# Performance work log

Hardware: AMD Instinct MI355X
Metric: run time of the kernel (lower is better)

## Reference

```python
import jax, jax.numpy as jnp
import numpy as np

B, T, D, H = 64, 4096, 256, 341  # hidden = 4*256//3 = 341
TAU, RHO, TV_W = 1.0, 0.3, 0.1
NEG = -1e9
EPS = 1e-6
LN_EPS = 1e-5


def entmax15(x, axis=-1):
    """Exact 1.5-entmax via the sort-based threshold algorithm (Peters et al.)."""
    x = (x - jnp.max(x, axis=axis, keepdims=True)) / 2.0
    xsrt = -jnp.sort(-x, axis=axis)                       # descending
    n = x.shape[axis]
    rho = jnp.arange(1, n + 1, dtype=x.dtype)
    mean = jnp.cumsum(xsrt, axis=axis) / rho
    mean_sq = jnp.cumsum(xsrt * xsrt, axis=axis) / rho
    ss = rho * (mean_sq - mean * mean)
    delta = (1.0 - ss) / rho
    tau = mean - jnp.sqrt(jnp.maximum(delta, 0.0))
    support = jnp.sum((tau <= xsrt).astype(jnp.int32), axis=axis, keepdims=True)
    tau_star = jnp.take_along_axis(tau, support - 1, axis=axis)
    return jnp.square(jnp.maximum(x - tau_star, 0.0))


def setup_inputs() -> dict:
    key = jax.random.key(0)
    k_emb, k_len, k_w1, k_w2 = jax.random.split(key, 4)
    embeddings = jax.random.normal(k_emb, (B, T, D), dtype=jnp.float32)
    # variable-length 0/1 attention mask (lengths in [T//4, T]) -> variable k per row
    lengths = jax.random.randint(k_len, (B,), T // 4, T + 1)
    attn = (jnp.arange(T)[None, :] < lengths[:, None]).astype(jnp.float32)
    ln_gamma = jnp.ones((D,), dtype=jnp.float32)
    ln_beta = jnp.zeros((D,), dtype=jnp.float32)
    W1 = jax.random.normal(k_w1, (D, H), dtype=jnp.float32) / np.sqrt(D)
    b1 = jnp.zeros((H,), dtype=jnp.float32)
    W2 = jax.random.normal(k_w2, (H,), dtype=jnp.float32) / np.sqrt(H)
    b2 = jnp.zeros((), dtype=jnp.float32)
    return {"embeddings": embeddings, "attn": attn, "ln_gamma": ln_gamma,
            "ln_beta": ln_beta, "W1": W1, "b1": b1, "W2": W2, "b2": b2}


def reference(embeddings, attn, ln_gamma, ln_beta, W1, b1, W2, b2):
    # SelectorMLP (dropout off at inference)
    emb = embeddings * attn[..., None]                              # [B,T,D]
    mu = jnp.mean(emb, axis=-1, keepdims=True)
    var = jnp.var(emb, axis=-1, keepdims=True)
    xn = (emb - mu) / jnp.sqrt(var + LN_EPS) * ln_gamma + ln_beta
    hid = jax.nn.gelu(jnp.einsum('btd,dh->bth', xn, W1) + b1, approximate=False)
    scores = jnp.einsum('bth,h->bt', hid, W2) + b2                  # [B,T]
    scores = jnp.where(attn == 0, NEG, scores)

    z = entmax15(scores / TAU, axis=1) * attn                       # soft rationale

    # probabilistic_top_k: gumbel-perturbed variable-k top-k, vectorized
    u = jax.random.uniform(jax.random.key(42), scores.shape, dtype=scores.dtype)
    gumbel = -jnp.log(-jnp.log(u + EPS) + EPS)
    pert = scores * attn + gumbel                                   # [B,T]
    t_eff = jnp.sum(attn, axis=1)                                   # [B]
    k = jnp.clip(jnp.round(RHO * t_eff), 1.0, jnp.maximum(t_eff, 1.0)).astype(jnp.int32)
    srt = -jnp.sort(-pert, axis=1)                                  # descending
    thr = jnp.take_along_axis(srt, (k - 1)[:, None], axis=1)        # k-th largest
    h = (pert >= thr).astype(z.dtype) * attn                        # hard mask

    # straight-through estimator
    g = jax.lax.stop_gradient(h - z) + z

    # total variation regularizer on g within valid region
    dz = jnp.abs(g[:, 1:] - g[:, :-1])
    valid = attn[:, 1:] * attn[:, :-1]
    tv = jnp.mean(jnp.sum(dz * valid, axis=1) / jnp.maximum(jnp.sum(valid, axis=1), 1.0))
    reg = TV_W * tv
    return (z, g, reg)
```

## Files before the change

### kernel.cpp

```cpp
#include <hip/hip_runtime.h>
#include <stdint.h>

#define BB 64
#define TT 4096
#define DD 256
#define HH 341
#define HP 384
#define NEGV (-1e9f)

typedef __attribute__((ext_vector_type(8))) short short8;
typedef __attribute__((ext_vector_type(4))) float f32x4;


__device__ inline float gelu_exact(float x) {
  return 0.5f * x * (1.0f + erff(x * 0.70710678118654752440f));
}

__device__ inline uint32_t rotl32(uint32_t x, int d) { return (x << d) | (x >> (32 - d)); }

__device__ inline uint32_t threefry_bits(uint32_t j) {
  const uint32_t K0 = 0u, K1 = 42u;
  const uint32_t K2 = K0 ^ K1 ^ 0x1BD11BDAu;
  uint32_t x0 = 0u, x1 = j;
  x0 += K0; x1 += K1;
#define TF_RND(r) { x0 += x1; x1 = rotl32(x1, r); x1 ^= x0; }
  TF_RND(13) TF_RND(15) TF_RND(26) TF_RND(6)
  x0 += K1; x1 += K2 + 1u;
  TF_RND(17) TF_RND(29) TF_RND(16) TF_RND(24)
  x0 += K2; x1 += K0 + 2u;
  TF_RND(13) TF_RND(15) TF_RND(26) TF_RND(6)
  x0 += K0; x1 += K1 + 3u;
  TF_RND(17) TF_RND(29) TF_RND(16) TF_RND(24)
  x0 += K1; x1 += K2 + 4u;
  TF_RND(13) TF_RND(15) TF_RND(26) TF_RND(6)
  x0 += K2; x1 += K0 + 5u;
#undef TF_RND
  return x0 ^ x1;
}

__device__ inline void bf16split(float x, short& hi, short& lo) {
  uint32_t u = __float_as_uint(x);
  uint32_t h = (u + 0x7FFFu + ((u >> 16) & 1u)) >> 16;
  float rem = x - __uint_as_float(h << 16);
  uint32_t ur = __float_as_uint(rem);
  uint32_t l = (ur + 0x7FFFu + ((ur >> 16) & 1u)) >> 16;
  hi = (short)h; lo = (short)l;
}

__device__ inline float bred_sum(float v, volatile float* tmp, int tid) {
#pragma unroll
  for (int o = 32; o; o >>= 1) v += __shfl_xor(v, o, 64);
  __syncthreads();
  if ((tid & 63) == 0) tmp[tid >> 6] = v;
  __syncthreads();
  return tmp[0] + tmp[1] + tmp[2] + tmp[3];
}

__device__ inline float bred_max(float v, volatile float* tmp, int tid) {
#pragma unroll
  for (int o = 32; o; o >>= 1) v = fmaxf(v, __shfl_xor(v, o, 64));
  __syncthreads();
  if ((tid & 63) == 0) tmp[tid >> 6] = v;
  __syncthreads();
  return fmaxf(fmaxf(tmp[0], tmp[1]), fmaxf(tmp[2], tmp[3]));
}

__device__ inline int bred_sum_i(int v, volatile int* tmp, int tid) {
#pragma unroll
  for (int o = 32; o; o >>= 1) v += __shfl_xor(v, o, 64);
  __syncthreads();
  if ((tid & 63) == 0) tmp[tid >> 6] = v;
  __syncthreads();
  return tmp[0] + tmp[1] + tmp[2] + tmp[3];
}


__global__ __launch_bounds__(256) void k0_prep(const float* __restrict__ W1,
                                               short* __restrict__ Whi,
                                               short* __restrict__ Wlo) {
  int idx = blockIdx.x * 256 + threadIdx.x;
  int h = idx >> 8, k = idx & 255;
  float v = (h < HH) ? W1[k * HH + h] : 0.0f;
  short hi, lo;
  bf16split(v, hi, lo);
  Whi[idx] = hi;
  Wlo[idx] = lo;
}


__global__ __launch_bounds__(256, 2) void k1_mfma(
    const float* __restrict__ emb, const float* __restrict__ attn,
    const float* __restrict__ gamma, const float* __restrict__ beta,
    const short* __restrict__ Whi, const float* __restrict__ b1,
    const float* __restrict__ W2, const float* __restrict__ b2,
    float* __restrict__ scores) {
  __shared__ short Ahi[16384];
  __shared__ short Alo[16384];

  const int bid = blockIdx.x;
  const int b = bid >> 6;
  const int t0 = (bid & 63) * 64;
  const int tid = threadIdx.x;
  const int w = tid >> 6;
  const int lane = tid & 63;

  if (attn[(size_t)b * TT + t0] == 0.0f) {
    if (tid < 64) scores[(size_t)b * TT + t0 + tid] = NEGV;
    return;
  }

  {
    const int half = lane >> 5;
    const int g = lane & 31;
    const int k0g = g >> 2, qg = g & 3;
    float gg[8], bb[8];
#pragma unroll
    for (int j = 0; j < 8; ++j) { gg[j] = gamma[g * 8 + j]; bb[j] = beta[g * 8 + j]; }

    for (int it = 0; it < 8; ++it) {
      const int il = w * 16 + it * 2 + half;
      const size_t rowoff = (size_t)b * TT + t0 + il;
      const float a = attn[rowoff];
      const float* ep = emb + rowoff * DD + g * 8;
      float x[8];
      {
        float4 xA = *(const float4*)ep;
        float4 xB = *(const float4*)(ep + 4);
        x[0] = xA.x * a; x[1] = xA.y * a; x[2] = xA.z * a; x[3] = xA.w * a;
        x[4] = xB.x * a; x[5] = xB.y * a; x[6] = xB.z * a; x[7] = xB.w * a;
      }
      float s = 0.f, ss = 0.f;
#pragma unroll
      for (int j = 0; j < 8; ++j) { s += x[j]; ss += x[j] * x[j]; }
#pragma unroll
      for (int o = 16; o; o >>= 1) { s += __shfl_xor(s, o, 32); ss += __shfl_xor(ss, o, 32); }
      const float mu = s * (1.0f / DD);
      const float rs = 1.0f / sqrtf(ss * (1.0f / DD) - mu * mu + 1e-5f);

      short8 h8, l8;
#pragma unroll
      for (int j = 0; j < 8; ++j) {
        float y = (x[j] - mu) * rs * gg[j] + bb[j];
        short hi, lo;
        bf16split(y, hi, lo);
        h8[j] = hi; l8[j] = lo;
      }
      const int i15 = it * 2 + half;
      const int slot = w * 512 + k0g * 64 + qg * 16 + (i15 ^ k0g);
      *(short8*)&Ahi[slot * 8] = h8;
      *(short8*)&Alo[slot * 8] = l8;
    }
  }
  __syncthreads();

  const int r = lane & 15, q = lane >> 4;
  f32x4 acc[6][4];
#pragma unroll
  for (int j = 0; j < 6; ++j)
#pragma unroll
    for (int mt = 0; mt < 4; ++mt) acc[j][mt] = (f32x4){0.f, 0.f, 0.f, 0.f};

  int hb[6];
#pragma unroll
  for (int j = 0; j < 6; ++j) hb[j] = ((w * 6 + j) * 16 + r) * 256 + q * 8;

  for (int k0 = 0; k0 < 8; ++k0) {
    short8 ahi[4], alo[4];
#pragma unroll
    for (int mt = 0; mt < 4; ++mt) {
      const int slot = mt * 512 + k0 * 64 + q * 16 + (r ^ k0);
      ahi[mt] = *(const short8*)&Ahi[slot * 8];
      alo[mt] = *(const short8*)&Alo[slot * 8];
    }
#pragma unroll
    for (int j = 0; j < 6; ++j) {
      const short* bp = Whi + hb[j] + k0 * 32;
      short8 bhi = *(const short8*)bp;
      short8 blo = *(const short8*)(bp + HP * DD);
#pragma unroll
      for (int mt = 0; mt < 4; ++mt) {
        acc[j][mt] = __builtin_amdgcn_mfma_f32_16x16x32_bf16(ahi[mt], bhi, acc[j][mt], 0, 0, 0);
        acc[j][mt] = __builtin_amdgcn_mfma_f32_16x16x32_bf16(ahi[mt], blo, acc[j][mt], 0, 0, 0);
        acc[j][mt] = __builtin_amdgcn_mfma_f32_16x16x32_bf16(alo[mt], bhi, acc[j][mt], 0, 0, 0);
      }
    }
  }

  float sacc[4][4];
#pragma unroll
  for (int mt = 0; mt < 4; ++mt)
#pragma unroll
    for (int rr = 0; rr < 4; ++rr) sacc[mt][rr] = 0.f;

#pragma unroll
  for (int j = 0; j < 6; ++j) {
    const int h = (w * 6 + j) * 16 + r;
    const float w2v = (h < HH) ? W2[h] : 0.f;
    const float b1v = (h < HH) ? b1[h] : 0.f;
#pragma unroll
    for (int mt = 0; mt < 4; ++mt)
#pragma unroll
      for (int rr = 0; rr < 4; ++rr) {
        float v = gelu_exact(acc[j][mt][rr] + b1v) * w2v;
        v += __shfl_xor(v, 1, 64);
        v += __shfl_xor(v, 2, 64);
        v += __shfl_xor(v, 4, 64);
        v += __shfl_xor(v, 8, 64);
        sacc[mt][rr] += v;
      }
  }

  __syncthreads();
  float* sred = (float*)Ahi;
  if (r == 0) {
#pragma unroll
    for (int mt = 0; mt < 4; ++mt)
#pragma unroll
      for (int rr = 0; rr < 4; ++rr)
        sred[w * 64 + mt * 16 + q * 4 + rr] = sacc[mt][rr];
  }
  __syncthreads();

  if (tid < 64) {
    float sc = sred[tid] + sred[64 + tid] + sred[128 + tid] + sred[192 + tid] + b2[0];
    float a = attn[(size_t)b * TT + t0 + tid];
    scores[(size_t)b * TT + t0 + tid] = (a != 0.f) ? sc : NEGV;
  }
}


__global__ __launch_bounds__(256) void k2_select(
    const float* __restrict__ attn, float* __restrict__ out, float* __restrict__ row_tv) {
  __shared__ float gs[TT];
  __shared__ float ftmp[4];
  __shared__ int itmp[4];

  const int b = blockIdx.x, tid = threadIdx.x;
  const float* arow = attn + (size_t)b * TT;
  float* zrow = out + (size_t)b * TT;
  float* grow = out + (size_t)BB * TT + (size_t)b * TT;

  float x_loc[16], a_loc[16];
  uint32_t key_loc[16];
  float cnt = 0.0f, mx = -3.4e38f;
#pragma unroll
  for (int i = 0; i < 16; ++i) {
    int t = tid + i * 256;
    float s = grow[t];
    float a = arow[t];
    a_loc[i] = a;
    x_loc[i] = s;
    cnt += a;
    mx = fmaxf(mx, s);
    uint32_t bits = threefry_bits((uint32_t)(b * TT + t));
    float u = __uint_as_float(0x3F800000u | (bits >> 9)) - 1.0f;
    float gum = -logf(1e-6f - logf(u + 1e-6f));
    float pert = (a != 0.0f ? s : 0.0f) + gum;
    uint32_t fb = __float_as_uint(pert);
    uint32_t msk = ((int32_t)fb < 0) ? 0xFFFFFFFFu : 0x80000000u;
    key_loc[i] = fb ^ msk;
  }
  float t_eff = bred_sum(cnt, ftmp, tid);
  mx = bred_max(mx, ftmp, tid);

#pragma unroll
  for (int i = 0; i < 16; ++i) x_loc[i] = (x_loc[i] - mx) * 0.5f;

  float lo = -1.0f, hi = 0.0f;
  for (int it = 0; it < 36; ++it) {
    float mid = 0.5f * (lo + hi);
    float p = 0.0f;
#pragma unroll
    for (int i = 0; i < 16; ++i) {
      float d = x_loc[i] - mid;
      if (d > 0.0f) p = fmaf(d, d, p);
    }
    float f = bred_sum(p, ftmp, tid);
    if (f >= 1.0f) lo = mid; else hi = mid;
  }
  const float tau = 0.5f * (lo + hi);

  float kf = rintf(0.3f * t_eff);
  kf = fminf(fmaxf(kf, 1.0f), fmaxf(t_eff, 1.0f));
  int kk = (int)kf;

  uint32_t prefix = 0u;
  for (int bit = 31; bit >= 0; --bit) {
    uint32_t test = prefix | (1u << bit);
    uint32_t hi_test = test >> bit;
    int c = 0;
#pragma unroll
    for (int i = 0; i < 16; ++i) c += (int)((key_loc[i] >> bit) == hi_test);
    int ct = bred_sum_i(c, itmp, tid);
    if (ct >= kk) prefix = test; else kk -= ct;
  }
  const uint32_t thr = prefix;

#pragma unroll
  for (int i = 0; i < 16; ++i) {
    int t = tid + i * 256;
    float d = x_loc[i] - tau;
    float z = (d > 0.0f) ? d * d : 0.0f;
    z *= a_loc[i];
    float h = (key_loc[i] >= thr) ? a_loc[i] : 0.0f;
    float g = (h - z) + z;
    zrow[t] = z;
    gs[t] = g;
  }
  __syncthreads();

  float tvn = 0.0f, tvd = 0.0f;
#pragma unroll
  for (int i = 0; i < 16; ++i) {
    int t = tid + i * 256;
    grow[t] = gs[t];
    if (t > 0) {
      float valid = arow[t] * arow[t - 1];
      tvn += fabsf(gs[t] - gs[t - 1]) * valid;
      tvd += valid;
    }
  }
  tvn = bred_sum(tvn, ftmp, tid);
  tvd = bred_sum(tvd, ftmp, tid);
  if (tid == 0) row_tv[b] = tvn / fmaxf(tvd, 1.0f);
}


__global__ __launch_bounds__(64) void k3_final(const float* __restrict__ row_tv,
                                               float* __restrict__ out) {
  float v = row_tv[threadIdx.x];
#pragma unroll
  for (int o = 32; o; o >>= 1) v += __shfl_xor(v, o, 64);
  if (threadIdx.x == 0) out[2 * BB * TT] = 0.1f * (v * (1.0f / BB));
}


extern "C" void kernel_launch(void* const* d_in, const int* in_sizes, int n_in,
                              void* d_out, int out_size, void* d_ws, size_t ws_size,
                              hipStream_t stream) {
  const float* emb   = (const float*)d_in[0];
  const float* attn  = (const float*)d_in[1];
  const float* gamma = (const float*)d_in[2];
  const float* beta  = (const float*)d_in[3];
  const float* W1    = (const float*)d_in[4];
  const float* b1    = (const float*)d_in[5];
  const float* W2    = (const float*)d_in[6];
  const float* b2    = (const float*)d_in[7];
  float* out = (float*)d_out;

  float* row_tv = (float*)d_ws;
  short* Whi = (short*)((char*)d_ws + 512);
  short* Wlo = Whi + HP * DD;

  k0_prep<<<dim3(HP * DD / 256), dim3(256), 0, stream>>>(W1, Whi, Wlo);
  k1_mfma<<<dim3(BB * TT / 64), dim3(256), 0, stream>>>(
      emb, attn, gamma, beta, Whi, b1, W2, b2, out + (size_t)BB * TT);
  k2_select<<<dim3(BB), dim3(256), 0, stream>>>(attn, out, row_tv);
  k3_final<<<dim3(1), dim3(64), 0, stream>>>(row_tv, out);
}
```

Measured before the change: 690.2 us.

## Widen MLP kernel to 512 threads, fast GELU, Newton entmax and radix-4 select

The MLP kernel now uses 8 waves per 64-token tile. Each wave owns 3 hidden-column tiles instead of 6, and the cross-lane shuffle reduction runs once per output instead of once per column tile. Exact erff GELU is replaced by an Abramowitz–Stegun polynomial using rcp and fast exp. In the selection kernel, the 36-step bisection for the entmax threshold becomes 18 clamped Newton steps with a fused two-value reduction, and the 32-step bitwise radix select becomes a 16-step radix-4 select with three counts reduced together. These cut ALU work and the number of block barriers, at the cost of small approximation error in GELU and a hard clamp on tau that assumes the threshold stays below -1/64.

```diff
diff --git a/kernel.cpp b/kernel.cpp
--- a/kernel.cpp
+++ b/kernel.cpp
@@ -12,8 +12,18 @@
 typedef __attribute__((ext_vector_type(4))) float f32x4;
 
 
-__device__ inline float gelu_exact(float x) {
-  return 0.5f * x * (1.0f + erff(x * 0.70710678118654752440f));
+__device__ inline float gelu_fast(float x) {
+  const float y = fabsf(x) * 0.70710678118654752440f;
+  const float t = __builtin_amdgcn_rcpf(fmaf(0.3275911f, y, 1.0f));
+  float p = fmaf(1.061405429f, t, -1.453152027f);
+  p = fmaf(p, t, 1.421413741f);
+  p = fmaf(p, t, -0.284496736f);
+  p = fmaf(p, t, 0.254829592f);
+  p *= t;
+  const float e = __expf(-y * y);
+  float er = fmaf(-p, e, 1.0f);
+  er = (x < 0.0f) ? -er : er;
+  return 0.5f * x * (1.0f + er);
 }
 
 __device__ inline uint32_t rotl32(uint32_t x, int d) { return (x << d) | (x >> (32 - d)); }
@@ -65,13 +75,29 @@
   return fmaxf(fmaxf(tmp[0], tmp[1]), fmaxf(tmp[2], tmp[3]));
 }
 
-__device__ inline int bred_sum_i(int v, volatile int* tmp, int tid) {
-#pragma unroll
-  for (int o = 32; o; o >>= 1) v += __shfl_xor(v, o, 64);
-  __syncthreads();
-  if ((tid & 63) == 0) tmp[tid >> 6] = v;
-  __syncthreads();
-  return tmp[0] + tmp[1] + tmp[2] + tmp[3];
+__device__ inline void bred_sum2(float& a, float& b, volatile float* tmp, int tid) {
+#pragma unroll
+  for (int o = 32; o; o >>= 1) { a += __shfl_xor(a, o, 64); b += __shfl_xor(b, o, 64); }
+  __syncthreads();
+  if ((tid & 63) == 0) { int w2 = (tid >> 6) * 2; tmp[w2] = a; tmp[w2 + 1] = b; }
+  __syncthreads();
+  a = tmp[0] + tmp[2] + tmp[4] + tmp[6];
+  b = tmp[1] + tmp[3] + tmp[5] + tmp[7];
+}
+
+__device__ inline void bred3_i(int& a, int& b, int& c, volatile int* tmp, int tid) {
+#pragma unroll
+  for (int o = 32; o; o >>= 1) {
+    a += __shfl_xor(a, o, 64);
+    b += __shfl_xor(b, o, 64);
+    c += __shfl_xor(c, o, 64);
+  }
+  __syncthreads();
+  if ((tid & 63) == 0) { int w3 = (tid >> 6) * 3; tmp[w3] = a; tmp[w3 + 1] = b; tmp[w3 + 2] = c; }
+  __syncthreads();
+  a = tmp[0] + tmp[3] + tmp[6] + tmp[9];
+  b = tmp[1] + tmp[4] + tmp[7] + tmp[10];
+  c = tmp[2] + tmp[5] + tmp[8] + tmp[11];
 }
 
 
@@ -88,7 +114,7 @@
 }
 
 
-__global__ __launch_bounds__(256, 2) void k1_mfma(
+__global__ __launch_bounds__(512, 4) void k1_mfma(
     const float* __restrict__ emb, const float* __restrict__ attn,
     const float* __restrict__ gamma, const float* __restrict__ beta,
     const short* __restrict__ Whi, const float* __restrict__ b1,
@@ -117,8 +143,8 @@
 #pragma unroll
     for (int j = 0; j < 8; ++j) { gg[j] = gamma[g * 8 + j]; bb[j] = beta[g * 8 + j]; }
 
-    for (int it = 0; it < 8; ++it) {
-      const int il = w * 16 + it * 2 + half;
+    for (int it = 0; it < 4; ++it) {
+      const int il = w * 8 + it * 2 + half;
       const size_t rowoff = (size_t)b * TT + t0 + il;
       const float a = attn[rowoff];
       const float* ep = emb + rowoff * DD + g * 8;
@@ -145,8 +171,8 @@
         bf16split(y, hi, lo);
         h8[j] = hi; l8[j] = lo;
       }
-      const int i15 = it * 2 + half;
-      const int slot = w * 512 + k0g * 64 + qg * 16 + (i15 ^ k0g);
+      const int i15 = il & 15, mt = il >> 4;
+      const int slot = mt * 512 + k0g * 64 + qg * 16 + (i15 ^ k0g);
       *(short8*)&Ahi[slot * 8] = h8;
       *(short8*)&Alo[slot * 8] = l8;
     }
@@ -154,15 +180,15 @@
   __syncthreads();
 
   const int r = lane & 15, q = lane >> 4;
-  f32x4 acc[6][4];
-#pragma unroll
-  for (int j = 0; j < 6; ++j)
+  f32x4 acc[3][4];
+#pragma unroll
+  for (int j = 0; j < 3; ++j)
 #pragma unroll
     for (int mt = 0; mt < 4; ++mt) acc[j][mt] = (f32x4){0.f, 0.f, 0.f, 0.f};
 
-  int hb[6];
-#pragma unroll
-  for (int j = 0; j < 6; ++j) hb[j] = ((w * 6 + j) * 16 + r) * 256 + q * 8;
+  int hb[3];
+#pragma unroll
+  for (int j = 0; j < 3; ++j) hb[j] = ((w * 3 + j) * 16 + r) * 256 + q * 8;
 
   for (int k0 = 0; k0 < 8; ++k0) {
     short8 ahi[4], alo[4];
@@ -173,7 +199,7 @@
       alo[mt] = *(const short8*)&Alo[slot * 8];
     }
 #pragma unroll
-    for (int j = 0; j < 6; ++j) {
+    for (int j = 0; j < 3; ++j) {
       const short* bp = Whi + hb[j] + k0 * 32;
       short8 bhi = *(const short8*)bp;
       short8 blo = *(const short8*)(bp + HP * DD);
@@ -186,29 +212,36 @@
     }
   }
 
-  float sacc[4][4];
+  float part[4][4];
 #pragma unroll
   for (int mt = 0; mt < 4; ++mt)
 #pragma unroll
-    for (int rr = 0; rr < 4; ++rr) sacc[mt][rr] = 0.f;
-
-#pragma unroll
-  for (int j = 0; j < 6; ++j) {
-    const int h = (w * 6 + j) * 16 + r;
+    for (int rr = 0; rr < 4; ++rr) part[mt][rr] = 0.f;
+
+#pragma unroll
+  for (int j = 0; j < 3; ++j) {
+    const int h = (w * 3 + j) * 16 + r;
     const float w2v = (h < HH) ? W2[h] : 0.f;
     const float b1v = (h < HH) ? b1[h] : 0.f;
 #pragma unroll
     for (int mt = 0; mt < 4; ++mt)
 #pragma unroll
-      for (int rr = 0; rr < 4; ++rr) {
-        float v = gelu_exact(acc[j][mt][rr] + b1v) * w2v;
-        v += __shfl_xor(v, 1, 64);
-        v += __shfl_xor(v, 2, 64);
-        v += __shfl_xor(v, 4, 64);
-        v += __shfl_xor(v, 8, 64);
-        sacc[mt][rr] += v;
-      }
-  }
+      for (int rr = 0; rr < 4; ++rr)
+        part[mt][rr] += gelu_fast(acc[j][mt][rr] + b1v) * w2v;
+  }
+
+  float sacc[4][4];
+#pragma unroll
+  for (int mt = 0; mt < 4; ++mt)
+#pragma unroll
+    for (int rr = 0; rr < 4; ++rr) {
+      float v = part[mt][rr];
+      v += __shfl_xor(v, 1, 64);
+      v += __shfl_xor(v, 2, 64);
+      v += __shfl_xor(v, 4, 64);
+      v += __shfl_xor(v, 8, 64);
+      sacc[mt][rr] = v;
+    }
 
   __syncthreads();
   float* sred = (float*)Ahi;
@@ -222,7 +255,9 @@
   __syncthreads();
 
   if (tid < 64) {
-    float sc = sred[tid] + sred[64 + tid] + sred[128 + tid] + sred[192 + tid] + b2[0];
+    float sc = b2[0];
+#pragma unroll
+    for (int ww = 0; ww < 8; ++ww) sc += sred[ww * 64 + tid];
     float a = attn[(size_t)b * TT + t0 + tid];
     scores[(size_t)b * TT + t0 + tid] = (a != 0.f) ? sc : NEGV;
   }
@@ -232,8 +267,8 @@
 __global__ __launch_bounds__(256) void k2_select(
     const float* __restrict__ attn, float* __restrict__ out, float* __restrict__ row_tv) {
   __shared__ float gs[TT];
-  __shared__ float ftmp[4];
-  __shared__ int itmp[4];
+  __shared__ float ftmp[8];
+  __shared__ int itmp[12];
 
   const int b = blockIdx.x, tid = threadIdx.x;
   const float* arow = attn + (size_t)b * TT;
@@ -266,33 +301,42 @@
 #pragma unroll
   for (int i = 0; i < 16; ++i) x_loc[i] = (x_loc[i] - mx) * 0.5f;
 
-  float lo = -1.0f, hi = 0.0f;
-  for (int it = 0; it < 36; ++it) {
-    float mid = 0.5f * (lo + hi);
-    float p = 0.0f;
+  float tau = -1.0f;
+  for (int it = 0; it < 18; ++it) {
+    float f = 0.0f, g = 0.0f;
 #pragma unroll
     for (int i = 0; i < 16; ++i) {
-      float d = x_loc[i] - mid;
-      if (d > 0.0f) p = fmaf(d, d, p);
-    }
-    float f = bred_sum(p, ftmp, tid);
-    if (f >= 1.0f) lo = mid; else hi = mid;
-  }
-  const float tau = 0.5f * (lo + hi);
+      float d = x_loc[i] - tau;
+      if (d > 0.0f) { f = fmaf(d, d, f); g += d; }
+    }
+    bred_sum2(f, g, ftmp, tid);
+    tau = fminf(tau + (f - 1.0f) / (2.0f * g), -0.015625f);
+  }
 
   float kf = rintf(0.3f * t_eff);
   kf = fminf(fmaxf(kf, 1.0f), fmaxf(t_eff, 1.0f));
   int kk = (int)kf;
 
   uint32_t prefix = 0u;
-  for (int bit = 31; bit >= 0; --bit) {
-    uint32_t test = prefix | (1u << bit);
-    uint32_t hi_test = test >> bit;
-    int c = 0;
-#pragma unroll
-    for (int i = 0; i < 16; ++i) c += (int)((key_loc[i] >> bit) == hi_test);
-    int ct = bred_sum_i(c, itmp, tid);
-    if (ct >= kk) prefix = test; else kk -= ct;
+  for (int bit = 30; bit >= 0; bit -= 2) {
+    uint32_t ph = (prefix >> 2) >> bit;
+    int c1 = 0, c2 = 0, c3 = 0;
+#pragma unroll
+    for (int i = 0; i < 16; ++i) {
+      uint32_t kb = key_loc[i];
+      bool m = (((kb >> 2) >> bit) == ph);
+      uint32_t d = (kb >> bit) & 3u;
+      c1 += (int)(m && d >= 1u);
+      c2 += (int)(m && d >= 2u);
+      c3 += (int)(m && d == 3u);
+    }
+    bred3_i(c1, c2, c3, itmp, tid);
+    uint32_t dig;
+    if (c3 >= kk) dig = 3u;
+    else if (c2 >= kk) { dig = 2u; kk -= c3; }
+    else if (c1 >= kk) { dig = 1u; kk -= c2; }
+    else { dig = 0u; kk -= c1; }
+    prefix |= dig << bit;
   }
   const uint32_t thr = prefix;
 
@@ -353,7 +397,7 @@
   short* Wlo = Whi + HP * DD;
 
   k0_prep<<<dim3(HP * DD / 256), dim3(256), 0, stream>>>(W1, Whi, Wlo);
-  k1_mfma<<<dim3(BB * TT / 64), dim3(256), 0, stream>>>(
+  k1_mfma<<<dim3(BB * TT / 64), dim3(512), 0, stream>>>(
       emb, attn, gamma, beta, Whi, b1, W2, b2, out + (size_t)BB * TT);
   k2_select<<<dim3(BB), dim3(256), 0, stream>>>(attn, out, row_tv);
   k3_final<<<dim3(1), dim3(64), 0, stream>>>(row_tv, out);
```

Result: faster. 553.6 us (-19.8%).
